# Performance work log

Measured on AMD Instinct MI355X. Metric: run time of the kernel, lower is better.

The kernel has to match this reference:

```python
import jax, jax.numpy as jnp
import numpy as np

L = 16384      # sequence length
D_IN = 512     # d_input
D_H = 1024     # d_hidden
D_OUT = 512    # d_output
R_MIN = 0.0
R_MAX = 0.99
MAX_PHASE = np.pi


def setup_inputs() -> dict:
    key = jax.random.key(0)
    k_nu, k_th, k_x, k_bre, k_bim, k_cre, k_cim, k_d = jax.random.split(key, 8)
    # nu_init with parametrization='exp'
    u_nu = jax.random.uniform(k_nu, (D_H,), dtype=jnp.float32)
    nu = jnp.sqrt(u_nu * (R_MAX ** 2 - R_MIN ** 2) + R_MIN ** 2)
    u_theta = jax.random.uniform(k_th, (D_H,), dtype=jnp.float32, minval=-MAX_PHASE, maxval=MAX_PHASE)
    theta = jnp.mod(u_theta, 2 * jnp.pi)
    lamb = jnp.stack([jnp.log(-jnp.log(nu)), jnp.log(theta)], axis=0)  # [2, D_H]
    # gamma_init with parametrization='exp': nu = exp(-exp(lamb[0]))
    nu_eff = jnp.exp(-jnp.exp(lamb[0]))
    gamma = jnp.log(jnp.sqrt(1.0 - jnp.abs(nu_eff) ** 2))  # [D_H]
    # matrix_init: normal / sqrt(shape[0])
    B_re = jax.random.normal(k_bre, (D_H, D_IN), dtype=jnp.float32) / jnp.sqrt(D_H)
    B_im = jax.random.normal(k_bim, (D_H, D_IN), dtype=jnp.float32) / jnp.sqrt(D_H)
    C_re = jax.random.normal(k_cre, (D_OUT, D_H), dtype=jnp.float32) / jnp.sqrt(D_OUT)
    C_im = jax.random.normal(k_cim, (D_OUT, D_H), dtype=jnp.float32) / jnp.sqrt(D_OUT)
    D = jax.random.normal(k_d, (D_OUT, D_IN), dtype=jnp.float32) / jnp.sqrt(D_OUT)
    inputs = jax.random.normal(k_x, (L, D_IN), dtype=jnp.float32)
    return {"inputs": inputs, "lamb": lamb, "gamma": gamma,
            "B_re": B_re, "B_im": B_im, "C_re": C_re, "C_im": C_im, "D": D}


def _binary_operator_diag(q_i, q_j):
    A_i, b_i = q_i
    A_j, b_j = q_j
    return (A_j * A_i, A_j * b_i + b_j)


def reference(inputs, lamb, gamma, B_re, B_im, C_re, C_im, D):
    # parametrization='exp': lambda = exp(-exp(nu_log) + i*exp(theta_log))
    diag_lambda = jnp.exp(-jnp.exp(lamb[0]) + 1j * jnp.exp(lamb[1]))  # [D_H] complex64
    # which_gamma='learned', exp param: scale rows of B by exp(gamma)
    B_norm = jnp.exp(gamma)[:, None] * (B_re + 1j * B_im)             # [D_H, D_IN]
    # Bu_t = B_norm @ x_t for all t, as one GEMM: [L, D_H] complex
    Bu = inputs.astype(B_norm.dtype) @ B_norm.T
    Lambda_elements = jnp.broadcast_to(diag_lambda[None, :], Bu.shape)
    # diagonal linear recurrence h_t = lambda*h_{t-1} + Bu_t via parallel scan
    _, h = jax.lax.associative_scan(_binary_operator_diag, (Lambda_elements, Bu))
    C = C_re + 1j * C_im
    # y_t = Re[C h_t] + D x_t
    outputs = jnp.real(h @ C.T) + inputs @ D.T  # [L, D_OUT]
    return outputs
```

## Files before the change

### kernel.cpp

```cpp
#include <hip/hip_runtime.h>

__device__ __forceinline__ unsigned short f2b(float f) {
    unsigned int u = __builtin_bit_cast(unsigned int, f);
    unsigned int r = (u + 0x7FFFu + ((u >> 16) & 1u)) >> 16;
    return (unsigned short)r;
}
__device__ __forceinline__ float b2f(unsigned short s) {
    unsigned int u = ((unsigned int)s) << 16;
    return __builtin_bit_cast(float, u);
}

typedef __attribute__((ext_vector_type(8))) short short8;
typedef __attribute__((ext_vector_type(4))) float float4v;

#define GLD16(g, l) __builtin_amdgcn_global_load_lds(                          \
    (const __attribute__((address_space(1))) unsigned int*)(g),                \
    (__attribute__((address_space(3))) unsigned int*)(l), 16, 0, 0)

#define WAIT_VMN(n) __builtin_amdgcn_s_waitcnt(0x0F70 | (n))
#define SB()        __builtin_amdgcn_sched_barrier(0)
#define BAR()       __builtin_amdgcn_s_barrier()

#define SEQLEN 16384
#define NCHUNK 512
#define TCHUNK 32
#define LDH 2560

__global__ void prep_all(const float* __restrict__ x,
                         const float* __restrict__ B_re, const float* __restrict__ B_im,
                         const float* __restrict__ gamma,
                         const float* __restrict__ C_re, const float* __restrict__ C_im,
                         const float* __restrict__ Dm,
                         unsigned short* __restrict__ Hcat,
                         unsigned short* __restrict__ Bcat,
                         unsigned short* __restrict__ CW) {
    int b = blockIdx.x;
    if (b < 8192) {
        int id = b * 256 + threadIdx.x;
        int t = id >> 7;
        int k4 = (id & 127) << 2;
        float4 v = *(const float4*)(x + (long)t * 512 + k4);
        ushort4 o;
        o.x = f2b(v.x); o.y = f2b(v.y); o.z = f2b(v.z); o.w = f2b(v.w);
        *(ushort4*)(Hcat + (long)t * LDH + 2048 + k4) = o;
    } else if (b < 9216) {
        int id = (b - 8192) * 256 + threadIdx.x;
        int n = id >> 7;
        int k4 = (id & 127) << 2;
        const float* src = (n < 1024) ? (B_re + (long)n * 512) : (B_im + (long)(n - 1024) * 512);
        float g = expf(gamma[n & 1023]);
        float4 v = *(const float4*)(src + k4);
        ushort4 o;
        o.x = f2b(v.x * g); o.y = f2b(v.y * g); o.z = f2b(v.z * g); o.w = f2b(v.w * g);
        *(ushort4*)(Bcat + (long)n * 512 + k4) = o;
    } else {
        int id = (b - 9216) * 256 + threadIdx.x;
        int o = id / 640;
        int j4 = (id - o * 640) << 2;
        float4 v; float sgn = 1.0f;
        if (j4 < 1024) {
            v = *(const float4*)(C_re + (long)o * 1024 + j4);
        } else if (j4 < 2048) {
            v = *(const float4*)(C_im + (long)o * 1024 + (j4 - 1024));
            sgn = -1.0f;
        } else {
            v = *(const float4*)(Dm + (long)o * 512 + (j4 - 2048));
        }
        ushort4 w;
        w.x = f2b(v.x * sgn); w.y = f2b(v.y * sgn); w.z = f2b(v.z * sgn); w.w = f2b(v.w * sgn);
        *(ushort4*)(CW + (long)o * 2560 + j4) = w;
    }
}

template <int MREP, bool OUT_BF16>
__launch_bounds__(512, 2)
__global__ void gemm_8p(const unsigned short* __restrict__ A, int lda,
                        const unsigned short* __restrict__ B, int ldb,
                        void* __restrict__ Cout, int ldc, int Ktot,
                        int nbx_shift) {
    constexpr int BM  = MREP * 32;
    constexpr int ASH = BM * 64;
    constexpr int NA  = BM / 64;
    constexpr int GPT = NA + 4;
    __shared__ unsigned short sm[2][ASH + 16384] __attribute__((aligned(16)));

    const int tid  = threadIdx.x;
    const int lane = tid & 63;
    const int wid  = tid >> 6;
    const int wr   = wid >> 2;
    const int wc   = wid & 3;

    const int bid = blockIdx.x;
    const int xcd = bid & 7;
    const int g   = bid >> 3;
    const int bx  = g & ((1 << nbx_shift) - 1);
    const int by  = xcd * (gridDim.x >> (3 + nbx_shift)) + (g >> nbx_shift);
    const long m0 = (long)by * BM;
    const long n0 = (long)bx * 256;

    const int sr = lane >> 3;
    const int sc = ((lane & 7) ^ sr) << 3;
    const unsigned short* Agl = A + (m0 + sr) * (long)lda + sc;
    const unsigned short* Bgl = B + (n0 + sr) * (long)ldb + sc;

    const int fr = lane & 15;
    const int x7 = fr & 7;
    const int k0off = (((lane >> 4)    ) ^ x7) << 3;
    const int k1off = (((lane >> 4) + 4) ^ x7) << 3;

    float4v acc[MREP][4] = {};
    short8 fa[MREP / 2][2];
    short8 fb[4][2];

    auto stageB = [&](unsigned short* buf, long kt) {
        unsigned short* ldsB = buf + ASH + wid * 512;
        const unsigned short* gB = Bgl + kt;
#pragma unroll
        for (int i = 0; i < 4; i++)
            GLD16(gB + (long)(8 * (wid + 8 * i)) * ldb, ldsB + i * 4096);
    };
    auto stageA = [&](unsigned short* buf, long kt) {
        unsigned short* ldsA = buf + wid * 512;
        const unsigned short* gA = Agl + kt;
#pragma unroll
        for (int i = 0; i < NA; i++)
            GLD16(gA + (long)(8 * (wid + 8 * i)) * lda, ldsA + i * 4096);
    };
    auto ldA = [&](const unsigned short* buf, int mbase) {
#pragma unroll
        for (int i = 0; i < MREP / 2; i++) {
            const unsigned short* p = buf + (wr * (BM / 2) + (mbase + i) * 16 + fr) * 64;
            fa[i][0] = *(const short8*)(p + k0off);
            fa[i][1] = *(const short8*)(p + k1off);
        }
    };
    auto ldB = [&](const unsigned short* buf, int nbase) {
#pragma unroll
        for (int j = 0; j < 2; j++) {
            const unsigned short* p = buf + ASH + (wc * 64 + (nbase + j) * 16 + fr) * 64;
            fb[nbase + j][0] = *(const short8*)(p + k0off);
            fb[nbase + j][1] = *(const short8*)(p + k1off);
        }
    };
    auto mfmaQ = [&](int mbase, int nbase) {
        __builtin_amdgcn_s_setprio(1);
#pragma unroll
        for (int i = 0; i < MREP / 2; i++)
#pragma unroll
            for (int j = 0; j < 2; j++) {
                acc[mbase + i][nbase + j] = __builtin_amdgcn_mfma_f32_16x16x32_bf16(
                    fa[i][0], fb[nbase + j][0], acc[mbase + i][nbase + j], 0, 0, 0);
                acc[mbase + i][nbase + j] = __builtin_amdgcn_mfma_f32_16x16x32_bf16(
                    fa[i][1], fb[nbase + j][1], acc[mbase + i][nbase + j], 0, 0, 0);
            }
        __builtin_amdgcn_s_setprio(0);
    };

    const int nk = Ktot >> 6;

    stageB(sm[0], 0);  stageA(sm[0], 0);
    stageB(sm[1], 64); stageA(sm[1], 64);
    WAIT_VMN(GPT);
    SB(); BAR(); SB();

    for (int t = 0; t < nk; ++t) {
        unsigned short* cur = sm[t & 1];
        const bool st = (t + 2 < nk);
        const long kt2 = (long)(t + 2) * 64;
        ldA(cur, 0); ldB(cur, 0);
        SB(); BAR(); SB();
        mfmaQ(0, 0);
        SB(); BAR(); SB();
        ldB(cur, 2);
        SB(); BAR(); SB();
        mfmaQ(0, 2);
        SB(); BAR(); SB();
        if (st) stageB(cur, kt2);
        ldA(cur, MREP / 2);
        SB(); BAR(); SB();
        mfmaQ(MREP / 2, 0);
        SB(); BAR(); SB();
        if (st) stageA(cur, kt2);
        SB();
        mfmaQ(MREP / 2, 2);
        if (st)              WAIT_VMN(GPT);
        else if (t + 1 < nk) WAIT_VMN(0);
        SB(); BAR(); SB();
    }

    const int er = (lane >> 4) * 4;
    const int ec = lane & 15;
#pragma unroll
    for (int mi = 0; mi < MREP; mi++) {
#pragma unroll
        for (int r = 0; r < 4; r++) {
            long grow = m0 + wr * (BM / 2) + mi * 16 + er + r;
#pragma unroll
            for (int nj = 0; nj < 4; nj++) {
                long gcol = n0 + wc * 64 + nj * 16 + ec;
                float v = acc[mi][nj][r];
                if (OUT_BF16)
                    ((unsigned short*)Cout)[grow * ldc + gcol] = f2b(v);
                else
                    ((float*)Cout)[grow * ldc + gcol] = v;
            }
        }
    }
}

__global__ void scan_ends(const unsigned short* __restrict__ Hcat,
                          const float* __restrict__ lamb,
                          float* __restrict__ E) {
    const int chunk = blockIdx.x;
    const int ch = threadIdx.x << 2;
    float lre[4], lim[4];
#pragma unroll
    for (int i = 0; i < 4; i++) {
        float nu = expf(-expf(lamb[ch + i]));
        float th = expf(lamb[1024 + ch + i]);
        lre[i] = nu * cosf(th);
        lim[i] = nu * sinf(th);
    }
    float hr[4] = {0, 0, 0, 0}, hi[4] = {0, 0, 0, 0};
    const unsigned short* base = Hcat + (long)chunk * TCHUNK * LDH + ch;
#pragma unroll 4
    for (int t = 0; t < TCHUNK; t++) {
        ushort4 br = *(const ushort4*)(base + (long)t * LDH);
        ushort4 bi = *(const ushort4*)(base + (long)t * LDH + 1024);
        float brf[4] = {b2f(br.x), b2f(br.y), b2f(br.z), b2f(br.w)};
        float bif[4] = {b2f(bi.x), b2f(bi.y), b2f(bi.z), b2f(bi.w)};
#pragma unroll
        for (int i = 0; i < 4; i++) {
            float nr = fmaf(lre[i], hr[i], fmaf(-lim[i], hi[i], brf[i]));
            float ni = fmaf(lre[i], hi[i], fmaf(lim[i], hr[i], bif[i]));
            hr[i] = nr; hi[i] = ni;
        }
    }
    float* Ec = E + (long)chunk * 2048 + ch;
#pragma unroll
    for (int i = 0; i < 4; i++) {
        Ec[i] = hr[i];
        Ec[1024 + i] = hi[i];
    }
}

__global__ void carry(const float* __restrict__ lamb, const float* __restrict__ E,
                      float* __restrict__ Kc) {
    const int ch = blockIdx.x * 256 + threadIdx.x;
    double nu = exp(-exp((double)lamb[ch]));
    double th = exp((double)lamb[1024 + ch]);
    double lr = nu * cos(th), li = nu * sin(th);
#pragma unroll
    for (int i = 0; i < 5; i++) {
        double rr = lr * lr - li * li;
        double ii = 2.0 * lr * li;
        lr = rr; li = ii;
    }
    float tre = (float)lr, tim = (float)li;
    float hr = 0.0f, hi = 0.0f;
#pragma unroll 8
    for (int c = 0; c < NCHUNK; c++) {
        Kc[(long)c * 2048 + ch] = hr;
        Kc[(long)c * 2048 + 1024 + ch] = hi;
        float er = E[(long)c * 2048 + ch];
        float ei = E[(long)c * 2048 + 1024 + ch];
        float nr = fmaf(tre, hr, fmaf(-tim, hi, er));
        float ni = fmaf(tre, hi, fmaf(tim, hr, ei));
        hr = nr; hi = ni;
    }
}

__global__ void scan_apply(unsigned short* __restrict__ Hcat,
                           const float* __restrict__ lamb,
                           const float* __restrict__ Kc) {
    const int chunk = blockIdx.x;
    const int ch = threadIdx.x << 2;
    float lre[4], lim[4];
#pragma unroll
    for (int i = 0; i < 4; i++) {
        float nu = expf(-expf(lamb[ch + i]));
        float th = expf(lamb[1024 + ch + i]);
        lre[i] = nu * cosf(th);
        lim[i] = nu * sinf(th);
    }
    float hr[4], hi[4];
#pragma unroll
    for (int i = 0; i < 4; i++) {
        hr[i] = Kc[(long)chunk * 2048 + ch + i];
        hi[i] = Kc[(long)chunk * 2048 + 1024 + ch + i];
    }
    unsigned short* base = Hcat + (long)chunk * TCHUNK * LDH + ch;
#pragma unroll 4
    for (int t = 0; t < TCHUNK; t++) {
        ushort4 br = *(const ushort4*)(base + (long)t * LDH);
        ushort4 bi = *(const ushort4*)(base + (long)t * LDH + 1024);
        float brf[4] = {b2f(br.x), b2f(br.y), b2f(br.z), b2f(br.w)};
        float bif[4] = {b2f(bi.x), b2f(bi.y), b2f(bi.z), b2f(bi.w)};
#pragma unroll
        for (int i = 0; i < 4; i++) {
            float nr = fmaf(lre[i], hr[i], fmaf(-lim[i], hi[i], brf[i]));
            float ni = fmaf(lre[i], hi[i], fmaf(lim[i], hr[i], bif[i]));
            hr[i] = nr; hi[i] = ni;
        }
        ushort4 orv, oiv;
        orv.x = f2b(hr[0]); orv.y = f2b(hr[1]); orv.z = f2b(hr[2]); orv.w = f2b(hr[3]);
        oiv.x = f2b(hi[0]); oiv.y = f2b(hi[1]); oiv.z = f2b(hi[2]); oiv.w = f2b(hi[3]);
        *(ushort4*)(base + (long)t * LDH) = orv;
        *(ushort4*)(base + (long)t * LDH + 1024) = oiv;
    }
}

extern "C" void kernel_launch(void* const* d_in, const int* in_sizes, int n_in,
                              void* d_out, int out_size, void* d_ws, size_t ws_size,
                              hipStream_t stream) {
    const float* x     = (const float*)d_in[0];
    const float* lamb  = (const float*)d_in[1];
    const float* gamma = (const float*)d_in[2];
    const float* B_re  = (const float*)d_in[3];
    const float* B_im  = (const float*)d_in[4];
    const float* C_re  = (const float*)d_in[5];
    const float* C_im  = (const float*)d_in[6];
    const float* Dm    = (const float*)d_in[7];

    char* ws = (char*)d_ws;
    unsigned short* Hcat = (unsigned short*)ws;
    float* E  = (float*)(ws + 83886080);
    float* Kc = E + (long)NCHUNK * 2048;
    unsigned short* Bcat = (unsigned short*)((char*)Kc + 4194304);
    unsigned short* CW   = Bcat + (long)2048 * 512;

    prep_all<<<10496, 256, 0, stream>>>(x, B_re, B_im, gamma, C_re, C_im, Dm, Hcat, Bcat, CW);
    gemm_8p<8, true><<<512, 512, 0, stream>>>(Hcat + 2048, LDH, Bcat, 512, Hcat, LDH, 512,
                                              3);
    scan_ends<<<NCHUNK, 256, 0, stream>>>(Hcat, lamb, E);
    carry<<<4, 256, 0, stream>>>(lamb, E, Kc);
    scan_apply<<<NCHUNK, 256, 0, stream>>>(Hcat, lamb, Kc);
    gemm_8p<4, false><<<256, 512, 0, stream>>>(Hcat, LDH, CW, 2560, (float*)d_out, 512, 2560,
                                               1);
}
```

Before: 263.7 us.

## Parallelize carry propagation with warp-level scan and streamline MREP=4 GEMM loop

The carry kernel previously ran a serial loop over 512 chunks with only 1024 threads across 4 blocks. It now assigns one wavefront per channel: each lane processes 8 chunks, lanes combine via a shuffle-based Hillis-Steele scan using lambda^256 powers, then each lane replays its 8 chunks. This trades a long serial dependency chain for more parallel work, possibly with slightly different float rounding. Separately, the MREP=4 GEMM path loads all A fragments at once and issues both global stages together, using fewer barriers per K step.

```diff
diff --git a/kernel.cpp b/kernel.cpp
--- a/kernel.cpp
+++ b/kernel.cpp
@@ -17,9 +17,10 @@
     (const __attribute__((address_space(1))) unsigned int*)(g),                \
     (__attribute__((address_space(3))) unsigned int*)(l), 16, 0, 0)
 
-#define WAIT_VMN(n) __builtin_amdgcn_s_waitcnt(0x0F70 | (n))
-#define SB()        __builtin_amdgcn_sched_barrier(0)
-#define BAR()       __builtin_amdgcn_s_barrier()
+#define WAIT_VMN(n)  __builtin_amdgcn_s_waitcnt(0x0F70 | (n))
+#define WAIT_LGKM0() __builtin_amdgcn_s_waitcnt(0xC07F)
+#define SB()         __builtin_amdgcn_sched_barrier(0)
+#define BAR()        __builtin_amdgcn_s_barrier()
 
 #define SEQLEN 16384
 #define NCHUNK 512
@@ -109,7 +110,7 @@
     const int k1off = (((lane >> 4) + 4) ^ x7) << 3;
 
     float4v acc[MREP][4] = {};
-    short8 fa[MREP / 2][2];
+    short8 fa[4][2];
     short8 fb[4][2];
 
     auto stageB = [&](unsigned short* buf, long kt) {
@@ -126,14 +127,6 @@
         for (int i = 0; i < NA; i++)
             GLD16(gA + (long)(8 * (wid + 8 * i)) * lda, ldsA + i * 4096);
     };
-    auto ldA = [&](const unsigned short* buf, int mbase) {
-#pragma unroll
-        for (int i = 0; i < MREP / 2; i++) {
-            const unsigned short* p = buf + (wr * (BM / 2) + (mbase + i) * 16 + fr) * 64;
-            fa[i][0] = *(const short8*)(p + k0off);
-            fa[i][1] = *(const short8*)(p + k1off);
-        }
-    };
     auto ldB = [&](const unsigned short* buf, int nbase) {
 #pragma unroll
         for (int j = 0; j < 2; j++) {
@@ -142,19 +135,6 @@
             fb[nbase + j][1] = *(const short8*)(p + k1off);
         }
     };
-    auto mfmaQ = [&](int mbase, int nbase) {
-        __builtin_amdgcn_s_setprio(1);
-#pragma unroll
-        for (int i = 0; i < MREP / 2; i++)
-#pragma unroll
-            for (int j = 0; j < 2; j++) {
-                acc[mbase + i][nbase + j] = __builtin_amdgcn_mfma_f32_16x16x32_bf16(
-                    fa[i][0], fb[nbase + j][0], acc[mbase + i][nbase + j], 0, 0, 0);
-                acc[mbase + i][nbase + j] = __builtin_amdgcn_mfma_f32_16x16x32_bf16(
-                    fa[i][1], fb[nbase + j][1], acc[mbase + i][nbase + j], 0, 0, 0);
-            }
-        __builtin_amdgcn_s_setprio(0);
-    };
 
     const int nk = Ktot >> 6;
 
@@ -163,29 +143,92 @@
     WAIT_VMN(GPT);
     SB(); BAR(); SB();
 
-    for (int t = 0; t < nk; ++t) {
-        unsigned short* cur = sm[t & 1];
-        const bool st = (t + 2 < nk);
-        const long kt2 = (long)(t + 2) * 64;
-        ldA(cur, 0); ldB(cur, 0);
-        SB(); BAR(); SB();
-        mfmaQ(0, 0);
-        SB(); BAR(); SB();
-        ldB(cur, 2);
-        SB(); BAR(); SB();
-        mfmaQ(0, 2);
-        SB(); BAR(); SB();
-        if (st) stageB(cur, kt2);
-        ldA(cur, MREP / 2);
-        SB(); BAR(); SB();
-        mfmaQ(MREP / 2, 0);
-        SB(); BAR(); SB();
-        if (st) stageA(cur, kt2);
-        SB();
-        mfmaQ(MREP / 2, 2);
-        if (st)              WAIT_VMN(GPT);
-        else if (t + 1 < nk) WAIT_VMN(0);
-        SB(); BAR(); SB();
+    if constexpr (MREP == 8) {
+        auto ldA = [&](const unsigned short* buf, int mbase) {
+#pragma unroll
+            for (int i = 0; i < 4; i++) {
+                const unsigned short* p = buf + (wr * 128 + (mbase + i) * 16 + fr) * 64;
+                fa[i][0] = *(const short8*)(p + k0off);
+                fa[i][1] = *(const short8*)(p + k1off);
+            }
+        };
+        auto mfmaQ = [&](int mbase, int nbase) {
+            __builtin_amdgcn_s_setprio(1);
+#pragma unroll
+            for (int i = 0; i < 4; i++)
+#pragma unroll
+                for (int j = 0; j < 2; j++) {
+                    acc[mbase + i][nbase + j] = __builtin_amdgcn_mfma_f32_16x16x32_bf16(
+                        fa[i][0], fb[nbase + j][0], acc[mbase + i][nbase + j], 0, 0, 0);
+                    acc[mbase + i][nbase + j] = __builtin_amdgcn_mfma_f32_16x16x32_bf16(
+                        fa[i][1], fb[nbase + j][1], acc[mbase + i][nbase + j], 0, 0, 0);
+                }
+            __builtin_amdgcn_s_setprio(0);
+        };
+        for (int t = 0; t < nk; ++t) {
+            unsigned short* cur = sm[t & 1];
+            const bool st = (t + 2 < nk);
+            const long kt2 = (long)(t + 2) * 64;
+            ldA(cur, 0); ldB(cur, 0);
+            SB(); BAR(); SB();
+            mfmaQ(0, 0);
+            SB(); BAR(); SB();
+            ldB(cur, 2);
+            SB(); BAR(); SB();
+            mfmaQ(0, 2);
+            SB(); BAR(); SB();
+            if (st) stageB(cur, kt2);
+            ldA(cur, 4);
+            SB(); BAR(); SB();
+            mfmaQ(4, 0);
+            SB(); BAR(); SB();
+            if (st) stageA(cur, kt2);
+            SB();
+            mfmaQ(4, 2);
+            if (st)              WAIT_VMN(GPT);
+            else if (t + 1 < nk) WAIT_VMN(0);
+            SB(); BAR(); SB();
+        }
+    } else {
+        auto ldAall = [&](const unsigned short* buf) {
+#pragma unroll
+            for (int i = 0; i < 4; i++) {
+                const unsigned short* p = buf + (wr * 64 + i * 16 + fr) * 64;
+                fa[i][0] = *(const short8*)(p + k0off);
+                fa[i][1] = *(const short8*)(p + k1off);
+            }
+        };
+        auto mfmaN2 = [&](int nbase) {
+            __builtin_amdgcn_s_setprio(1);
+#pragma unroll
+            for (int i = 0; i < 4; i++)
+#pragma unroll
+                for (int j = 0; j < 2; j++) {
+                    acc[i][nbase + j] = __builtin_amdgcn_mfma_f32_16x16x32_bf16(
+                        fa[i][0], fb[nbase + j][0], acc[i][nbase + j], 0, 0, 0);
+                    acc[i][nbase + j] = __builtin_amdgcn_mfma_f32_16x16x32_bf16(
+                        fa[i][1], fb[nbase + j][1], acc[i][nbase + j], 0, 0, 0);
+                }
+            __builtin_amdgcn_s_setprio(0);
+        };
+        for (int t = 0; t < nk; ++t) {
+            unsigned short* cur = sm[t & 1];
+            const bool st = (t + 2 < nk);
+            const long kt2 = (long)(t + 2) * 64;
+            ldAall(cur); ldB(cur, 0);
+            SB(); BAR(); SB();
+            mfmaN2(0);
+            SB(); BAR(); SB();
+            ldB(cur, 2);
+            WAIT_LGKM0();
+            SB(); BAR(); SB();
+            if (st) { stageB(cur, kt2); stageA(cur, kt2); }
+            SB();
+            mfmaN2(2);
+            if (st)              WAIT_VMN(GPT);
+            else if (t + 1 < nk) WAIT_VMN(0);
+            SB(); BAR(); SB();
+        }
     }
 
     const int er = (lane >> 4) * 4;
@@ -246,7 +289,8 @@
 
 __global__ void carry(const float* __restrict__ lamb, const float* __restrict__ E,
                       float* __restrict__ Kc) {
-    const int ch = blockIdx.x * 256 + threadIdx.x;
+    const int lane = threadIdx.x & 63;
+    const int ch = blockIdx.x * 4 + (threadIdx.x >> 6);
     double nu = exp(-exp((double)lamb[ch]));
     double th = exp((double)lamb[1024 + ch]);
     double lr = nu * cos(th), li = nu * sin(th);
@@ -256,17 +300,55 @@
         double ii = 2.0 * lr * li;
         lr = rr; li = ii;
     }
-    float tre = (float)lr, tim = (float)li;
+    const float tre = (float)lr, tim = (float)li;
+    double ar = lr, ai = li;
+#pragma unroll
+    for (int i = 0; i < 3; i++) {
+        double rr = ar * ar - ai * ai;
+        double ii = 2.0 * ar * ai;
+        ar = rr; ai = ii;
+    }
+    float Ar = (float)ar, Ai = (float)ai;
+
+    const int c0 = lane * 8;
+    float er[8], ei[8];
+#pragma unroll
+    for (int j = 0; j < 8; j++) {
+        er[j] = E[(long)(c0 + j) * 2048 + ch];
+        ei[j] = E[(long)(c0 + j) * 2048 + 1024 + ch];
+    }
     float hr = 0.0f, hi = 0.0f;
-#pragma unroll 8
-    for (int c = 0; c < NCHUNK; c++) {
-        Kc[(long)c * 2048 + ch] = hr;
-        Kc[(long)c * 2048 + 1024 + ch] = hi;
-        float er = E[(long)c * 2048 + ch];
-        float ei = E[(long)c * 2048 + 1024 + ch];
-        float nr = fmaf(tre, hr, fmaf(-tim, hi, er));
-        float ni = fmaf(tre, hi, fmaf(tim, hr, ei));
+#pragma unroll
+    for (int j = 0; j < 8; j++) {
+        float nr = fmaf(tre, hr, fmaf(-tim, hi, er[j]));
+        float ni = fmaf(tre, hi, fmaf(tim, hr, ei[j]));
         hr = nr; hi = ni;
+    }
+#pragma unroll
+    for (int o = 1; o < 64; o <<= 1) {
+        float pr = __shfl_up(hr, o);
+        float pi = __shfl_up(hi, o);
+        float qr = __shfl_up(Ar, o);
+        float qi = __shfl_up(Ai, o);
+        if (lane >= o) {
+            float nr = fmaf(Ar, pr, fmaf(-Ai, pi, hr));
+            float ni = fmaf(Ar, pi, fmaf(Ai, pr, hi));
+            hr = nr; hi = ni;
+            float nar = Ar * qr - Ai * qi;
+            float nai = Ar * qi + Ai * qr;
+            Ar = nar; Ai = nai;
+        }
+    }
+    float sr = __shfl_up(hr, 1);
+    float si = __shfl_up(hi, 1);
+    if (lane == 0) { sr = 0.0f; si = 0.0f; }
+#pragma unroll
+    for (int j = 0; j < 8; j++) {
+        Kc[(long)(c0 + j) * 2048 + ch] = sr;
+        Kc[(long)(c0 + j) * 2048 + 1024 + ch] = si;
+        float nr = fmaf(tre, sr, fmaf(-tim, si, er[j]));
+        float ni = fmaf(tre, si, fmaf(tim, sr, ei[j]));
+        sr = nr; si = ni;
     }
 }
 
@@ -333,7 +415,7 @@
     gemm_8p<8, true><<<512, 512, 0, stream>>>(Hcat + 2048, LDH, Bcat, 512, Hcat, LDH, 512,
                                               3);
     scan_ends<<<NCHUNK, 256, 0, stream>>>(Hcat, lamb, E);
-    carry<<<4, 256, 0, stream>>>(lamb, E, Kc);
+    carry<<<256, 256, 0, stream>>>(lamb, E, Kc);
     scan_apply<<<NCHUNK, 256, 0, stream>>>(Hcat, lamb, Kc);
     gemm_8p<4, false><<<256, 512, 0, stream>>>(Hcat, LDH, CW, 2560, (float*)d_out, 512, 2560,
                                                1);
```

Result: faster. 242.1 us (-8.2%).
